# Optimization experiments

Measured on AMD Instinct MI355X. Metric: run time of the kernel, lower is better.

## Reference

```python
import jax, jax.numpy as jnp
import numpy as np

DIM = 1024
HEADS = 16
EPS = 1e-5


def layer_norm(x, gamma, beta):
    mu = jnp.mean(x, axis=-1, keepdims=True)
    var = jnp.mean(jnp.square(x - mu), axis=-1, keepdims=True)
    return (x - mu) * jax.lax.rsqrt(var + EPS) * gamma + beta


def setup_inputs() -> dict:
    key = jax.random.key(0)
    ks = jax.random.split(key, 9)
    B, Nq, Nk = 8, 1024, 1024
    s = 1.0 / np.sqrt(DIM)
    return {
        "x": jax.random.normal(ks[0], (B, Nq, DIM), jnp.float32),
        "context": jax.random.normal(ks[1], (B, Nk, DIM), jnp.float32),
        "relative_position_bias": jax.random.normal(ks[2], (HEADS, Nq, Nk), jnp.float32),
        "Wq": jax.random.normal(ks[3], (DIM, DIM), jnp.float32) * s,
        "Wk": jax.random.normal(ks[4], (DIM, DIM), jnp.float32) * s,
        "Wv": jax.random.normal(ks[5], (DIM, DIM), jnp.float32) * s,
        "Wo": jax.random.normal(ks[6], (DIM, DIM), jnp.float32) * s,
        "bo": jnp.zeros((DIM,), jnp.float32),
        "gamma": jnp.ones((DIM,), jnp.float32),
        "beta": jnp.zeros((DIM,), jnp.float32),
    }


def reference(x, context, relative_position_bias, Wq, Wk, Wv, Wo, bo, gamma, beta):
    h = HEADS
    d = DIM // h
    scale = d ** -0.5
    xn = layer_norm(x, gamma, beta)
    cn = layer_norm(context, gamma, beta)
    B, Nq, _ = x.shape
    Nk = context.shape[1]
    # b n (h d) -> b h n d
    q = (xn @ Wq).reshape(B, Nq, h, d).transpose(0, 2, 1, 3)
    k = (cn @ Wk).reshape(B, Nk, h, d).transpose(0, 2, 1, 3)
    v = (cn @ Wv).reshape(B, Nk, h, d).transpose(0, 2, 1, 3)
    scores = jnp.einsum('bhid,bhjd->bhij', q, k) * scale
    scores = scores + relative_position_bias[None]
    attn = jax.nn.softmax(scores, axis=-1)
    out = jnp.einsum('bhij,bhjd->bhid', attn, v)
    out = out.transpose(0, 2, 1, 3).reshape(B, Nq, h * d)
    return out @ Wo + bo
```

## Files before the change

### kernel.cpp

```cpp
#include <hip/hip_runtime.h>
#include <hip/hip_bf16.h>
#include <stdint.h>

#define DIM   1024
#define HEADS 16
#define HD    64
#define NB    8
#define NTOK  1024
#define MROWS (NB*NTOK)

#define LOG2E 1.4426950408889634f
#define SCL   (0.125f * LOG2E)

typedef __attribute__((ext_vector_type(8))) _Float16 f16x8;
typedef __attribute__((ext_vector_type(4))) _Float16 f16x4;
typedef __attribute__((ext_vector_type(4))) float    f32x4;

typedef unsigned int uint_as1 __attribute__((address_space(1)));
typedef unsigned int uint_as3 __attribute__((address_space(3)));

__device__ __forceinline__ void gload16(const void* g, void* l) {
    __builtin_amdgcn_global_load_lds((const uint_as1*)g, (uint_as3*)l, 16, 0, 0);
}

__device__ __forceinline__ unsigned pkrtz(float a, float b) {
    auto h = __builtin_amdgcn_cvt_pkrtz(a, b);
    return __builtin_bit_cast(unsigned, h);
}

#if __has_builtin(__builtin_amdgcn_permlane32_swap)
__device__ __forceinline__ void swap32(unsigned& a, unsigned& b) {
    auto r = __builtin_amdgcn_permlane32_swap(a, b, false, false);
    a = r[0]; b = r[1];
}
#else
__device__ __forceinline__ void swap32(unsigned& a, unsigned& b) {
    unsigned as = (unsigned)__shfl_xor((int)a, 32, 64);
    unsigned bs = (unsigned)__shfl_xor((int)b, 32, 64);
    bool lo = ((threadIdx.x & 63) < 32);
    unsigned na = lo ? a : bs, nb = lo ? as : b;
    a = na; b = nb;
}
#endif
#if __has_builtin(__builtin_amdgcn_permlane16_swap)
__device__ __forceinline__ void swap16(unsigned& a, unsigned& b) {
    auto r = __builtin_amdgcn_permlane16_swap(a, b, false, false);
    a = r[0]; b = r[1];
}
#else
__device__ __forceinline__ void swap16(unsigned& a, unsigned& b) {
    unsigned as = (unsigned)__shfl_xor((int)a, 16, 64);
    unsigned bs = (unsigned)__shfl_xor((int)b, 16, 64);
    bool ev = ((threadIdx.x & 16) == 0);
    unsigned na = ev ? a : bs, nb = ev ? as : b;
    a = na; b = nb;
}
#endif
__device__ __forceinline__ float redsum32(float x) {
    unsigned a = __builtin_bit_cast(unsigned, x), b = a;
    swap32(a, b);
    return __builtin_bit_cast(float, a) + __builtin_bit_cast(float, b);
}
__device__ __forceinline__ float redsum16(float x) {
    unsigned a = __builtin_bit_cast(unsigned, x), b = a;
    swap16(a, b);
    return __builtin_bit_cast(float, a) + __builtin_bit_cast(float, b);
}

__global__ __launch_bounds__(256) void ln_kernel(const float* __restrict__ x,
                                                 const float* __restrict__ ctx,
                                                 const float* __restrict__ gamma,
                                                 const float* __restrict__ beta,
                                                 _Float16* __restrict__ xn,
                                                 _Float16* __restrict__ cn) {
    int row = blockIdx.x;
    const float* src; _Float16* dst;
    if (row < MROWS) { src = x + (size_t)row * DIM;          dst = xn + (size_t)row * DIM; }
    else             { int r = row - MROWS;
                       src = ctx + (size_t)r * DIM;          dst = cn + (size_t)r * DIM; }
    int t = threadIdx.x;
    float4 v = *(const float4*)(src + t * 4);
    float s  = v.x + v.y + v.z + v.w;
    float s2 = v.x*v.x + v.y*v.y + v.z*v.z + v.w*v.w;
    #pragma unroll
    for (int o = 32; o; o >>= 1) { s += __shfl_xor(s, o, 64); s2 += __shfl_xor(s2, o, 64); }
    __shared__ float red[8];
    int w = t >> 6, l = t & 63;
    if (l == 0) { red[w] = s; red[4 + w] = s2; }
    __syncthreads();
    s  = red[0] + red[1] + red[2] + red[3];
    s2 = red[4] + red[5] + red[6] + red[7];
    float mu   = s * (1.0f / DIM);
    float rstd = rsqrtf(s2 * (1.0f / DIM) - mu * mu + 1e-5f);
    float4 g  = *(const float4*)(gamma + t * 4);
    float4 bb = *(const float4*)(beta  + t * 4);
    f16x4 o;
    o[0] = (_Float16)((v.x - mu) * rstd * g.x + bb.x);
    o[1] = (_Float16)((v.y - mu) * rstd * g.y + bb.y);
    o[2] = (_Float16)((v.z - mu) * rstd * g.z + bb.z);
    o[3] = (_Float16)((v.w - mu) * rstd * g.w + bb.w);
    *(f16x4*)(dst + t * 4) = o;
}

__global__ __launch_bounds__(256) void biasconv_kernel(const float* __restrict__ bias,
                                                       _Float16* __restrict__ bias2) {
    size_t i = ((size_t)blockIdx.x * 256 + threadIdx.x) * 8;
    float4 a = *(const float4*)(bias + i);
    float4 b = *(const float4*)(bias + i + 4);
    f16x8 o;
    o[0] = (_Float16)(a.x * LOG2E); o[1] = (_Float16)(a.y * LOG2E);
    o[2] = (_Float16)(a.z * LOG2E); o[3] = (_Float16)(a.w * LOG2E);
    o[4] = (_Float16)(b.x * LOG2E); o[5] = (_Float16)(b.y * LOG2E);
    o[6] = (_Float16)(b.z * LOG2E); o[7] = (_Float16)(b.w * LOG2E);
    *(f16x8*)(bias2 + i) = o;
}

__global__ __launch_bounds__(256) void wtrans_kernel(const float* __restrict__ Wq, const float* __restrict__ Wk,
                                                     const float* __restrict__ Wv, const float* __restrict__ Wo,
                                                     _Float16* __restrict__ Tq, _Float16* __restrict__ Tk,
                                                     _Float16* __restrict__ Tv, _Float16* __restrict__ To) {
    __shared__ float tile[32][33];
    int m = blockIdx.z;
    const float* W = (m == 0) ? Wq : (m == 1) ? Wk : (m == 2) ? Wv : Wo;
    _Float16*    T = (m == 0) ? Tq : (m == 1) ? Tk : (m == 2) ? Tv : To;
    int j0 = blockIdx.x * 32, k0 = blockIdx.y * 32;
    int tx = threadIdx.x, ty = threadIdx.y;
    #pragma unroll
    for (int i = 0; i < 4; i++) tile[ty + i*8][tx] = W[(size_t)(k0 + ty + i*8) * DIM + j0 + tx];
    __syncthreads();
    #pragma unroll
    for (int i = 0; i < 4; i++) T[(size_t)(j0 + ty + i*8) * DIM + k0 + tx] = (_Float16)tile[tx][ty + i*8];
}

template<int MODE>
__global__ __launch_bounds__(256) void gemm_bt(const _Float16* __restrict__ A,
                                               const _Float16* __restrict__ BT,
                                               void* __restrict__ Cout,
                                               const float* __restrict__ bias) {
    __shared__ _Float16 As[128 * 64];
    __shared__ _Float16 Bs[128 * 64];
    const int K = DIM;
    int m0 = blockIdx.x * 128, n0 = blockIdx.y * 128;
    int t = threadIdx.x, w = t >> 6, l = t & 63;
    int wr = w >> 1, wc = w & 1, ln = l & 15, qtr = l >> 4;
    f32x4 acc[4][4] = {};
    int srow = w * 8 + (l >> 3);
    int cg   = (l & 7) ^ (srow & 7);
    const _Float16* Ag = A  + (size_t)(m0 + srow) * K + cg * 8;
    const _Float16* Bg = BT + (size_t)(n0 + srow) * K + cg * 8;
    for (int kt = 0; kt < K; kt += 64) {
        #pragma unroll
        for (int p = 0; p < 4; p++) {
            gload16(Ag + (size_t)(p * 32) * K, &As[(p * 32 + w * 8) * 64]);
            gload16(Bg + (size_t)(p * 32) * K, &Bs[(p * 32 + w * 8) * 64]);
        }
        Ag += 64; Bg += 64;
        __syncthreads();
        #pragma unroll
        for (int kk = 0; kk < 2; kk++) {
            f16x8 af[4], bfr[4];
            #pragma unroll
            for (int r = 0; r < 4; r++)
                af[r]  = *(const f16x8*)&As[(wr * 64 + r * 16 + ln) * 64 + (((qtr + kk*4) ^ (ln & 7)) * 8)];
            #pragma unroll
            for (int c = 0; c < 4; c++)
                bfr[c] = *(const f16x8*)&Bs[(wc * 64 + c * 16 + ln) * 64 + (((qtr + kk*4) ^ (ln & 7)) * 8)];
            #pragma unroll
            for (int r = 0; r < 4; r++)
                #pragma unroll
                for (int c = 0; c < 4; c++)
                    acc[r][c] = __builtin_amdgcn_mfma_f32_16x16x32_f16(af[r], bfr[c], acc[r][c], 0, 0, 0);
        }
        __syncthreads();
    }
    #pragma unroll
    for (int r = 0; r < 4; r++)
        #pragma unroll
        for (int c = 0; c < 4; c++) {
            int gn = n0 + wc * 64 + c * 16 + ln;
            #pragma unroll
            for (int q = 0; q < 4; q++) {
                int gm = m0 + wr * 64 + r * 16 + qtr * 4 + q;
                float v = acc[r][c][q];
                if constexpr (MODE == 0 || MODE == 1) {
                    int b = gm >> 10, n = gm & 1023, h = gn >> 6, d = gn & 63;
                    float sc = (MODE == 1) ? SCL : 1.0f;
                    ((_Float16*)Cout)[(((size_t)(b * HEADS + h) * NTOK + n) << 6) + d] = (_Float16)(v * sc);
                } else if constexpr (MODE == 2) {
                    int b = gm >> 10, n = gm & 1023, h = gn >> 6, d = gn & 63;
                    ((_Float16*)Cout)[(((size_t)(b * HEADS + h) * HD + d) << 10) + n] = (_Float16)v;
                } else {
                    ((float*)Cout)[(size_t)gm * DIM + gn] = v + bias[gn];
                }
            }
        }
}

__global__ __launch_bounds__(256) void attn_kernel(const _Float16* __restrict__ qb,
                                                   const _Float16* __restrict__ kb,
                                                   const _Float16* __restrict__ vt,
                                                   const _Float16* __restrict__ bias2,
                                                   _Float16* __restrict__ ao) {
    __shared__ _Float16 Kt[2][64 * 64];
    __shared__ _Float16 Vs[2][64 * 64];
    int bid = blockIdx.x;
    int rem = bid >> 3;
    int h = (bid & 7) * 2 + (rem & 1);
    int b = (rem >> 1) & 7;
    int qt = rem >> 4;
    int q0 = qt * 128;
    int t = threadIdx.x, w = t >> 6, l = t & 63, ln = l & 15, qtr = l >> 4;
    const _Float16* qbase = qb + (size_t)(b * HEADS + h) * NTOK * HD;
    const _Float16* kbase = kb + (size_t)(b * HEADS + h) * NTOK * HD;
    const _Float16* vbase = vt + (size_t)(b * HEADS + h) * HD * NTOK;
    const _Float16* bbase = bias2 + ((size_t)h * NTOK + q0 + w * 32) * NTOK;

    f16x8 qfr[2][2];
    #pragma unroll
    for (int qf = 0; qf < 2; qf++)
        #pragma unroll
        for (int ks = 0; ks < 2; ks++)
            qfr[qf][ks] = *(const f16x8*)&qbase[(size_t)(q0 + w*32 + qf*16 + ln) * HD + ks*32 + qtr*8];

#define STAGE(BUF, J0) do {                                                     \
        int rb_ = w * 16;                                                       \
        _Float16* kl_ = &Kt[BUF][rb_ * 64];                                     \
        _Float16* vl_ = &Vs[BUF][rb_ * 64];                                     \
        int r_ = rb_ + (l >> 3); int cg_ = (l & 7) ^ (r_ & 7);                  \
        gload16(kbase + (size_t)((J0) + r_) * HD + cg_ * 8, kl_);               \
        gload16(vbase + (size_t)r_ * NTOK + (J0) + cg_ * 8, vl_);               \
        r_ += 8; cg_ = (l & 7) ^ (r_ & 7);                                      \
        gload16(kbase + (size_t)((J0) + r_) * HD + cg_ * 8, kl_ + 8 * 64);      \
        gload16(vbase + (size_t)r_ * NTOK + (J0) + cg_ * 8, vl_ + 8 * 64);      \
    } while (0)

#define LOADB(DST, TT) do {                                                     \
        _Pragma("unroll")                                                       \
        for (int qf_ = 0; qf_ < 2; qf_++)                                       \
            _Pragma("unroll")                                                   \
            for (int r_ = 0; r_ < 4; r_++)                                      \
                DST[qf_][r_] = *(const f16x4*)&bbase[(size_t)(qf_*16 + ln) * NTOK \
                                                     + (TT)*64 + qtr*4 + r_*16]; \
    } while (0)

    STAGE(0, 0);
    f16x4 bpp[2][2][4];
    LOADB(bpp[0], 0);
    __syncthreads();

    float l_part[2] = {0.f, 0.f};
    f32x4 acc[2][4] = {};

    #pragma unroll 2
    for (int tt = 0; tt < 16; tt++) {
        int cur = tt & 1;
        if (tt < 15) { STAGE(cur ^ 1, (tt + 1) * 64); LOADB(bpp[cur ^ 1], tt + 1); }

        f32x4 st2[2][4];
        #pragma unroll
        for (int qf = 0; qf < 2; qf++)
            #pragma unroll
            for (int r = 0; r < 4; r++) {
                f16x4 bb = bpp[cur][qf][r];
                f32x4 ci = {(float)bb[0], (float)bb[1], (float)bb[2], (float)bb[3]};
                st2[qf][r] = ci;
            }
        __builtin_amdgcn_s_setprio(1);
        #pragma unroll
        for (int r = 0; r < 4; r++) {
            int row = r * 16 + ln;
            #pragma unroll
            for (int ks = 0; ks < 2; ks++) {
                f16x8 kf = *(const f16x8*)&Kt[cur][row * 64 + (((qtr + ks*4) ^ (ln & 7)) * 8)];
                st2[0][r] = __builtin_amdgcn_mfma_f32_16x16x32_f16(kf, qfr[0][ks], st2[0][r], 0, 0, 0);
                st2[1][r] = __builtin_amdgcn_mfma_f32_16x16x32_f16(kf, qfr[1][ks], st2[1][r], 0, 0, 0);
            }
        }
        __builtin_amdgcn_s_setprio(0);

        f16x8 pfr[2][2];
        #pragma unroll
        for (int qf = 0; qf < 2; qf++) {
            float sig = 0.f;
            unsigned pk2[4][2];
            #pragma unroll
            for (int r = 0; r < 4; r++) {
                float p0 = exp2f(st2[qf][r][0]);
                float p1 = exp2f(st2[qf][r][1]);
                float p2 = exp2f(st2[qf][r][2]);
                float p3 = exp2f(st2[qf][r][3]);
                sig += (p0 + p1) + (p2 + p3);
                pk2[r][0] = pkrtz(p0, p1);
                pk2[r][1] = pkrtz(p2, p3);
            }
            l_part[qf] += sig;

            #pragma unroll
            for (int ks = 0; ks < 2; ks++) {
                unsigned pw[4];
                #pragma unroll
                for (int c = 0; c < 2; c++) {
                    unsigned U = pk2[2*ks][c], T = pk2[2*ks + 1][c];
                    swap32(U, T);
                    swap16(U, T);
                    pw[c]     = U;
                    pw[2 + c] = T;
                }
                pfr[qf][ks] = __builtin_bit_cast(f16x8, *(const uint4*)pw);
            }
        }

        __builtin_amdgcn_s_setprio(1);
        #pragma unroll
        for (int dg = 0; dg < 4; dg++) {
            int row = dg * 16 + ln;
            #pragma unroll
            for (int ks = 0; ks < 2; ks++) {
                f16x8 vf = *(const f16x8*)&Vs[cur][row * 64 + (((qtr + ks*4) ^ (ln & 7)) * 8)];
                acc[0][dg] = __builtin_amdgcn_mfma_f32_16x16x32_f16(pfr[0][ks], vf, acc[0][dg], 0, 0, 0);
                acc[1][dg] = __builtin_amdgcn_mfma_f32_16x16x32_f16(pfr[1][ks], vf, acc[1][dg], 0, 0, 0);
            }
        }
        __builtin_amdgcn_s_setprio(0);
        __syncthreads();
    }

    #pragma unroll
    for (int qf = 0; qf < 2; qf++) {
        float inv = 1.0f / redsum16(redsum32(l_part[qf]));
        float invm[4];
        #pragma unroll
        for (int m = 0; m < 4; m++) invm[m] = __shfl(inv, (l & 48) | (qtr * 4 + m), 64);
        size_t rowb = (size_t)b * NTOK + q0 + w * 32 + qf * 16 + qtr * 4;
        #pragma unroll
        for (int dg = 0; dg < 4; dg++)
            #pragma unroll
            for (int m = 0; m < 4; m++)
                ao[(rowb + m) * DIM + h * HD + dg * 16 + ln] = (_Float16)(acc[qf][dg][m] * invm[m]);
    }
#undef STAGE
#undef LOADB
}

extern "C" void kernel_launch(void* const* d_in, const int* in_sizes, int n_in,
                              void* d_out, int out_size, void* d_ws, size_t ws_size,
                              hipStream_t stream) {
    const float* x     = (const float*)d_in[0];
    const float* ctx   = (const float*)d_in[1];
    const float* bias  = (const float*)d_in[2];
    const float* Wq    = (const float*)d_in[3];
    const float* Wk    = (const float*)d_in[4];
    const float* Wv    = (const float*)d_in[5];
    const float* Wo    = (const float*)d_in[6];
    const float* bo    = (const float*)d_in[7];
    const float* gamma = (const float*)d_in[8];
    const float* beta  = (const float*)d_in[9];
    float* out = (float*)d_out;

    _Float16* ws  = (_Float16*)d_ws;
    _Float16* xn  = ws;
    _Float16* cn  = xn  + (size_t)MROWS * DIM;
    _Float16* wqT = cn  + (size_t)MROWS * DIM;
    _Float16* wkT = wqT + (size_t)DIM * DIM;
    _Float16* wvT = wkT + (size_t)DIM * DIM;
    _Float16* woT = wvT + (size_t)DIM * DIM;
    _Float16* qbf = woT + (size_t)DIM * DIM;
    _Float16* kbf = qbf + (size_t)MROWS * DIM;
    _Float16* vtb = kbf + (size_t)MROWS * DIM;
    _Float16* aob = vtb + (size_t)MROWS * DIM;
    _Float16* bias2 = ws;

    ln_kernel<<<dim3(2 * MROWS), dim3(256), 0, stream>>>(x, ctx, gamma, beta, xn, cn);
    wtrans_kernel<<<dim3(32, 32, 4), dim3(32, 8), 0, stream>>>(Wq, Wk, Wv, Wo, wqT, wkT, wvT, woT);
    gemm_bt<1><<<dim3(64, 8), dim3(256), 0, stream>>>(xn, wqT, qbf, nullptr);
    gemm_bt<0><<<dim3(64, 8), dim3(256), 0, stream>>>(cn, wkT, kbf, nullptr);
    gemm_bt<2><<<dim3(64, 8), dim3(256), 0, stream>>>(cn, wvT, vtb, nullptr);
    biasconv_kernel<<<dim3(8192), dim3(256), 0, stream>>>(bias, bias2);
    attn_kernel<<<dim3(NB * HEADS * 8), dim3(256), 0, stream>>>(qbf, kbf, vtb, bias2, aob);
    gemm_bt<3><<<dim3(64, 8), dim3(256), 0, stream>>>(aob, woT, out, bo);
}
```

Before: 224.4 us.

## Fuse K and V projections into one GEMM and halve attention query tile

The K and V projection GEMMs become a single launch over a 2048-wide output by relying on wkT and wvT being contiguous in the workspace. The epilogue routes columns below 1024 to the K layout and the rest to the transposed V layout. The attention kernel now gives each wave 16 query rows instead of 32, which doubles the grid and halves per-wave registers and MFMA work. The aim is to cut a launch and raise occupancy and parallelism, at the cost of loading each K/V tile twice as often across blocks.

```diff
diff --git a/kernel.cpp b/kernel.cpp
--- a/kernel.cpp
+++ b/kernel.cpp
@@ -136,6 +136,7 @@
 __global__ __launch_bounds__(256) void gemm_bt(const _Float16* __restrict__ A,
                                                const _Float16* __restrict__ BT,
                                                void* __restrict__ Cout,
+                                               void* __restrict__ Cout2,
                                                const float* __restrict__ bias) {
     __shared__ _Float16 As[128 * 64];
     __shared__ _Float16 Bs[128 * 64];
@@ -189,6 +190,15 @@
                 } else if constexpr (MODE == 2) {
                     int b = gm >> 10, n = gm & 1023, h = gn >> 6, d = gn & 63;
                     ((_Float16*)Cout)[(((size_t)(b * HEADS + h) * HD + d) << 10) + n] = (_Float16)v;
+                } else if constexpr (MODE == 4) {
+                    int b = gm >> 10, n = gm & 1023;
+                    if (gn < 1024) {
+                        int h = gn >> 6, d = gn & 63;
+                        ((_Float16*)Cout)[(((size_t)(b * HEADS + h) * NTOK + n) << 6) + d] = (_Float16)v;
+                    } else {
+                        int g2 = gn - 1024, h = g2 >> 6, d = g2 & 63;
+                        ((_Float16*)Cout2)[(((size_t)(b * HEADS + h) * HD + d) << 10) + n] = (_Float16)v;
+                    }
                 } else {
                     ((float*)Cout)[(size_t)gm * DIM + gn] = v + bias[gn];
                 }
@@ -208,19 +218,17 @@
     int h = (bid & 7) * 2 + (rem & 1);
     int b = (rem >> 1) & 7;
     int qt = rem >> 4;
-    int q0 = qt * 128;
+    int q0 = qt * 64;
     int t = threadIdx.x, w = t >> 6, l = t & 63, ln = l & 15, qtr = l >> 4;
     const _Float16* qbase = qb + (size_t)(b * HEADS + h) * NTOK * HD;
     const _Float16* kbase = kb + (size_t)(b * HEADS + h) * NTOK * HD;
     const _Float16* vbase = vt + (size_t)(b * HEADS + h) * HD * NTOK;
-    const _Float16* bbase = bias2 + ((size_t)h * NTOK + q0 + w * 32) * NTOK;
-
-    f16x8 qfr[2][2];
-    #pragma unroll
-    for (int qf = 0; qf < 2; qf++)
-        #pragma unroll
-        for (int ks = 0; ks < 2; ks++)
-            qfr[qf][ks] = *(const f16x8*)&qbase[(size_t)(q0 + w*32 + qf*16 + ln) * HD + ks*32 + qtr*8];
+    const _Float16* bbase = bias2 + ((size_t)h * NTOK + q0 + w * 16) * NTOK;
+
+    f16x8 qfr[2];
+    #pragma unroll
+    for (int ks = 0; ks < 2; ks++)
+        qfr[ks] = *(const f16x8*)&qbase[(size_t)(q0 + w*16 + ln) * HD + ks*32 + qtr*8];
 
 #define STAGE(BUF, J0) do {                                                     \
         int rb_ = w * 16;                                                       \
@@ -236,35 +244,31 @@
 
 #define LOADB(DST, TT) do {                                                     \
         _Pragma("unroll")                                                       \
-        for (int qf_ = 0; qf_ < 2; qf_++)                                       \
-            _Pragma("unroll")                                                   \
-            for (int r_ = 0; r_ < 4; r_++)                                      \
-                DST[qf_][r_] = *(const f16x4*)&bbase[(size_t)(qf_*16 + ln) * NTOK \
-                                                     + (TT)*64 + qtr*4 + r_*16]; \
+        for (int r_ = 0; r_ < 4; r_++)                                          \
+            DST[r_] = *(const f16x4*)&bbase[(size_t)ln * NTOK                   \
+                                            + (TT)*64 + qtr*4 + r_*16];         \
     } while (0)
 
     STAGE(0, 0);
-    f16x4 bpp[2][2][4];
+    f16x4 bpp[2][4];
     LOADB(bpp[0], 0);
     __syncthreads();
 
-    float l_part[2] = {0.f, 0.f};
-    f32x4 acc[2][4] = {};
+    float l_part = 0.f;
+    f32x4 acc[4] = {};
 
     #pragma unroll 2
     for (int tt = 0; tt < 16; tt++) {
         int cur = tt & 1;
         if (tt < 15) { STAGE(cur ^ 1, (tt + 1) * 64); LOADB(bpp[cur ^ 1], tt + 1); }
 
-        f32x4 st2[2][4];
-        #pragma unroll
-        for (int qf = 0; qf < 2; qf++)
-            #pragma unroll
-            for (int r = 0; r < 4; r++) {
-                f16x4 bb = bpp[cur][qf][r];
-                f32x4 ci = {(float)bb[0], (float)bb[1], (float)bb[2], (float)bb[3]};
-                st2[qf][r] = ci;
-            }
+        f32x4 st2[4];
+        #pragma unroll
+        for (int r = 0; r < 4; r++) {
+            f16x4 bb = bpp[cur][r];
+            f32x4 ci = {(float)bb[0], (float)bb[1], (float)bb[2], (float)bb[3]};
+            st2[r] = ci;
+        }
         __builtin_amdgcn_s_setprio(1);
         #pragma unroll
         for (int r = 0; r < 4; r++) {
@@ -272,42 +276,38 @@
             #pragma unroll
             for (int ks = 0; ks < 2; ks++) {
                 f16x8 kf = *(const f16x8*)&Kt[cur][row * 64 + (((qtr + ks*4) ^ (ln & 7)) * 8)];
-                st2[0][r] = __builtin_amdgcn_mfma_f32_16x16x32_f16(kf, qfr[0][ks], st2[0][r], 0, 0, 0);
-                st2[1][r] = __builtin_amdgcn_mfma_f32_16x16x32_f16(kf, qfr[1][ks], st2[1][r], 0, 0, 0);
+                st2[r] = __builtin_amdgcn_mfma_f32_16x16x32_f16(kf, qfr[ks], st2[r], 0, 0, 0);
             }
         }
         __builtin_amdgcn_s_setprio(0);
 
-        f16x8 pfr[2][2];
-        #pragma unroll
-        for (int qf = 0; qf < 2; qf++) {
-            float sig = 0.f;
-            unsigned pk2[4][2];
-            #pragma unroll
-            for (int r = 0; r < 4; r++) {
-                float p0 = exp2f(st2[qf][r][0]);
-                float p1 = exp2f(st2[qf][r][1]);
-                float p2 = exp2f(st2[qf][r][2]);
-                float p3 = exp2f(st2[qf][r][3]);
-                sig += (p0 + p1) + (p2 + p3);
-                pk2[r][0] = pkrtz(p0, p1);
-                pk2[r][1] = pkrtz(p2, p3);
+        float sig = 0.f;
+        unsigned pk2[4][2];
+        #pragma unroll
+        for (int r = 0; r < 4; r++) {
+            float p0 = exp2f(st2[r][0]);
+            float p1 = exp2f(st2[r][1]);
+            float p2 = exp2f(st2[r][2]);
+            float p3 = exp2f(st2[r][3]);
+            sig += (p0 + p1) + (p2 + p3);
+            pk2[r][0] = pkrtz(p0, p1);
+            pk2[r][1] = pkrtz(p2, p3);
+        }
+        l_part += sig;
+
+        f16x8 pfr[2];
+        #pragma unroll
+        for (int ks = 0; ks < 2; ks++) {
+            unsigned pw[4];
+            #pragma unroll
+            for (int c = 0; c < 2; c++) {
+                unsigned U = pk2[2*ks][c], T = pk2[2*ks + 1][c];
+                swap32(U, T);
+                swap16(U, T);
+                pw[c]     = U;
+                pw[2 + c] = T;
             }
-            l_part[qf] += sig;
-
-            #pragma unroll
-            for (int ks = 0; ks < 2; ks++) {
-                unsigned pw[4];
-                #pragma unroll
-                for (int c = 0; c < 2; c++) {
-                    unsigned U = pk2[2*ks][c], T = pk2[2*ks + 1][c];
-                    swap32(U, T);
-                    swap16(U, T);
-                    pw[c]     = U;
-                    pw[2 + c] = T;
-                }
-                pfr[qf][ks] = __builtin_bit_cast(f16x8, *(const uint4*)pw);
-            }
+            pfr[ks] = __builtin_bit_cast(f16x8, *(const uint4*)pw);
         }
 
         __builtin_amdgcn_s_setprio(1);
@@ -317,27 +317,23 @@
             #pragma unroll
             for (int ks = 0; ks < 2; ks++) {
                 f16x8 vf = *(const f16x8*)&Vs[cur][row * 64 + (((qtr + ks*4) ^ (ln & 7)) * 8)];
-                acc[0][dg] = __builtin_amdgcn_mfma_f32_16x16x32_f16(pfr[0][ks], vf, acc[0][dg], 0, 0, 0);
-                acc[1][dg] = __builtin_amdgcn_mfma_f32_16x16x32_f16(pfr[1][ks], vf, acc[1][dg], 0, 0, 0);
+                acc[dg] = __builtin_amdgcn_mfma_f32_16x16x32_f16(pfr[ks], vf, acc[dg], 0, 0, 0);
             }
         }
         __builtin_amdgcn_s_setprio(0);
         __syncthreads();
     }
 
-    #pragma unroll
-    for (int qf = 0; qf < 2; qf++) {
-        float inv = 1.0f / redsum16(redsum32(l_part[qf]));
-        float invm[4];
-        #pragma unroll
-        for (int m = 0; m < 4; m++) invm[m] = __shfl(inv, (l & 48) | (qtr * 4 + m), 64);
-        size_t rowb = (size_t)b * NTOK + q0 + w * 32 + qf * 16 + qtr * 4;
-        #pragma unroll
-        for (int dg = 0; dg < 4; dg++)
-            #pragma unroll
-            for (int m = 0; m < 4; m++)
-                ao[(rowb + m) * DIM + h * HD + dg * 16 + ln] = (_Float16)(acc[qf][dg][m] * invm[m]);
-    }
+    float inv = 1.0f / redsum16(redsum32(l_part));
+    float invm[4];
+    #pragma unroll
+    for (int m = 0; m < 4; m++) invm[m] = __shfl(inv, (l & 48) | (qtr * 4 + m), 64);
+    size_t rowb = (size_t)b * NTOK + q0 + w * 16 + qtr * 4;
+    #pragma unroll
+    for (int dg = 0; dg < 4; dg++)
+        #pragma unroll
+        for (int m = 0; m < 4; m++)
+            ao[(rowb + m) * DIM + h * HD + dg * 16 + ln] = (_Float16)(acc[dg][m] * invm[m]);
 #undef STAGE
 #undef LOADB
 }
@@ -372,10 +368,9 @@
 
     ln_kernel<<<dim3(2 * MROWS), dim3(256), 0, stream>>>(x, ctx, gamma, beta, xn, cn);
     wtrans_kernel<<<dim3(32, 32, 4), dim3(32, 8), 0, stream>>>(Wq, Wk, Wv, Wo, wqT, wkT, wvT, woT);
-    gemm_bt<1><<<dim3(64, 8), dim3(256), 0, stream>>>(xn, wqT, qbf, nullptr);
-    gemm_bt<0><<<dim3(64, 8), dim3(256), 0, stream>>>(cn, wkT, kbf, nullptr);
-    gemm_bt<2><<<dim3(64, 8), dim3(256), 0, stream>>>(cn, wvT, vtb, nullptr);
+    gemm_bt<1><<<dim3(64, 8), dim3(256), 0, stream>>>(xn, wqT, qbf, nullptr, nullptr);
+    gemm_bt<4><<<dim3(64, 16), dim3(256), 0, stream>>>(cn, wkT, kbf, vtb, nullptr);
     biasconv_kernel<<<dim3(8192), dim3(256), 0, stream>>>(bias, bias2);
-    attn_kernel<<<dim3(NB * HEADS * 8), dim3(256), 0, stream>>>(qbf, kbf, vtb, bias2, aob);
-    gemm_bt<3><<<dim3(64, 8), dim3(256), 0, stream>>>(aob, woT, out, bo);
-}
+    attn_kernel<<<dim3(NB * HEADS * 16), dim3(256), 0, stream>>>(qbf, kbf, vtb, bias2, aob);
+    gemm_bt<3><<<dim3(64, 8), dim3(256), 0, stream>>>(aob, woT, out, nullptr, bo);
+}
```

Result: slower. 233.2 us (+3.9%).
